# Kernel optimization log

Hardware: AMD Instinct MI355X
Metric: run time of the kernel (lower is better)

## Reference

```python
import jax, jax.numpy as jnp
import numpy as np

B, S, D, H = 2, 2048, 1024, 16
HD = D // H  # head_dim = 64


def setup_inputs() -> dict:
    key = jax.random.key(0)
    ks = jax.random.split(key, 5)
    scale = 1.0 / np.sqrt(D)
    return {
        "x": jax.random.normal(ks[0], (B, S, D), dtype=jnp.float32),
        "attention_mask": jnp.zeros((B, 1, 1, S), dtype=jnp.float32),
        "Wq": jax.random.normal(ks[1], (D, D), dtype=jnp.float32) * scale,
        "Wk": jax.random.normal(ks[2], (D, D), dtype=jnp.float32) * scale,
        "Wv": jax.random.normal(ks[3], (D, D), dtype=jnp.float32) * scale,
        "Wo": jax.random.normal(ks[4], (D, D), dtype=jnp.float32) * scale,
    }


def reference(x, attention_mask, Wq, Wk, Wv, Wo):
    # nn.Linear applies x @ W.T; weights here stored as [out, in]
    q = jnp.einsum("bsd,ed->bse", x, Wq).reshape(B, S, H, HD).transpose(0, 2, 1, 3)
    k = jnp.einsum("bsd,ed->bse", x, Wk).reshape(B, S, H, HD).transpose(0, 2, 1, 3)
    v = jnp.einsum("bsd,ed->bse", x, Wv).reshape(B, S, H, HD).transpose(0, 2, 1, 3)
    scores = jnp.einsum("bhqd,bhkd->bhqk", q, k) / jnp.sqrt(jnp.float32(HD))
    scores = scores + attention_mask  # additive mask, broadcasts [B,1,1,S]
    attn = jax.nn.softmax(scores, axis=-1)  # dropout p=0 (eval) -> identity
    ctx = jnp.einsum("bhqk,bhkd->bhqd", attn, v)
    ctx = ctx.transpose(0, 2, 1, 3).reshape(B, S, D)
    out = jnp.einsum("bsd,ed->bse", ctx, Wo)
    return out
```

## Files before the change

### kernel.cpp

```cpp
#include <hip/hip_runtime.h>
#include <hip/hip_bf16.h>
#include <cstdint>
#include <cstddef>


#define B_  2
#define S_  2048
#define D_  1024
#define H_  16
#define HD_ 64

typedef __bf16 bf16x8 __attribute__((ext_vector_type(8)));
typedef __bf16 bf16x4 __attribute__((ext_vector_type(4)));
typedef float  f32x4  __attribute__((ext_vector_type(4)));

__device__ __forceinline__ void async16(const __bf16* g, const __bf16* l) {
  __builtin_amdgcn_global_load_lds(
      (const __attribute__((address_space(1))) void*)(uintptr_t)g,
      (__attribute__((address_space(3))) void*)(uint32_t)(uintptr_t)l,
      16, 0, 0);
}

__device__ __forceinline__ unsigned cvt_pk_bf16(float lo, float hi) {
  unsigned r;
  asm("v_cvt_pk_bf16_f32 %0, %1, %2" : "=v"(r) : "v"(lo), "v"(hi));
  return r;
}

__global__ __launch_bounds__(256) void cvt_all(const float* __restrict__ x,
    const float* __restrict__ wq, const float* __restrict__ wk,
    const float* __restrict__ wv, const float* __restrict__ wo,
    __bf16* __restrict__ xb, __bf16* __restrict__ wqb, __bf16* __restrict__ wkb,
    __bf16* __restrict__ wvb, __bf16* __restrict__ wob) {
  const int sel = blockIdx.y;
  const float* src; __bf16* dst; int n;
  if      (sel == 0) { src = x;  dst = xb;  n = B_ * S_ * D_; }
  else if (sel == 1) { src = wq; dst = wqb; n = D_ * D_; }
  else if (sel == 2) { src = wk; dst = wkb; n = D_ * D_; }
  else if (sel == 3) { src = wv; dst = wvb; n = D_ * D_; }
  else               { src = wo; dst = wob; n = D_ * D_; }
  for (int i = blockIdx.x * 256 + threadIdx.x; i * 4 < n; i += gridDim.x * 256) {
    const float4 v = *(const float4*)(src + (size_t)i * 4);
    bf16x4 o;
    o[0] = (__bf16)v.x; o[1] = (__bf16)v.y; o[2] = (__bf16)v.z; o[3] = (__bf16)v.w;
    *(bf16x4*)(dst + (size_t)i * 4) = o;
  }
}

template <typename TC>
__device__ __forceinline__ void gemm97_body(const __bf16* __restrict__ A,
                                            const __bf16* __restrict__ Bm,
                                            TC* __restrict__ C,
                                            const int m0, const int n0,
                                            const int N, const int K) {
  __shared__ __align__(16) __bf16 As[128 * 64];
  __shared__ __align__(16) __bf16 Bs[128 * 64];
  const int tid  = threadIdx.x, lane = tid & 63, wave = tid >> 6;
  const int l15  = lane & 15,   quad = lane >> 4;
  const int wr   = wave >> 1,   wc   = wave & 1;
  const int ebase = wave * 2048 + lane * 8;

  f32x4 acc[4][4] = {};
  for (int k0 = 0; k0 < K; k0 += 64) {
#pragma unroll
    for (int i = 0; i < 4; ++i) {
      const int e = ebase + i * 512;
      const int row = e >> 6, col = e & 63;
      async16(A  + (size_t)(m0 + row) * K + k0 + col, As + (wave * 4 + i) * 512);
      async16(Bm + (size_t)(n0 + row) * K + k0 + col, Bs + (wave * 4 + i) * 512);
    }
    __syncthreads();
#pragma unroll
    for (int kk = 0; kk < 2; ++kk) {
      bf16x8 af[4], bfv[4];
#pragma unroll
      for (int rt = 0; rt < 4; ++rt)
        af[rt] = *(const bf16x8*)(As + (wr * 64 + rt * 16 + l15) * 64 + kk * 32 + quad * 8);
#pragma unroll
      for (int ct = 0; ct < 4; ++ct)
        bfv[ct] = *(const bf16x8*)(Bs + (wc * 64 + ct * 16 + l15) * 64 + kk * 32 + quad * 8);
#pragma unroll
      for (int rt = 0; rt < 4; ++rt)
#pragma unroll
        for (int ct = 0; ct < 4; ++ct)
          acc[rt][ct] = __builtin_amdgcn_mfma_f32_16x16x32_bf16(af[rt], bfv[ct], acc[rt][ct], 0, 0, 0);
    }
    __syncthreads();
  }
#pragma unroll
  for (int rt = 0; rt < 4; ++rt)
#pragma unroll
    for (int ct = 0; ct < 4; ++ct)
#pragma unroll
      for (int r = 0; r < 4; ++r) {
        const int row = m0 + wr * 64 + rt * 16 + quad * 4 + r;
        const int col = n0 + wc * 64 + ct * 16 + l15;
        C[(size_t)row * N + col] = (TC)acc[rt][ct][r];
      }
}

__global__ __launch_bounds__(256) void qkv_gemm(const __bf16* __restrict__ xb,
                                                const __bf16* __restrict__ wq,
                                                const __bf16* __restrict__ wk,
                                                const __bf16* __restrict__ wv,
                                                __bf16* __restrict__ qkv) {
  __shared__ __align__(16) __bf16 As[128 * 64];
  __shared__ __align__(16) __bf16 Bs[128 * 64];
  __shared__ __align__(16) __bf16 cs[64 * 136];
  const int sel = blockIdx.x >> 3;
  const __bf16* Bm = (sel == 0) ? wq : (sel == 1) ? wk : wv;
  const int m0 = blockIdx.y * 128, n0 = (blockIdx.x & 7) * 128;
  constexpr int K = D_, N = D_;
  constexpr size_t NTE = (size_t)B_ * S_ * D_;

  const int tid  = threadIdx.x, lane = tid & 63, wave = tid >> 6;
  const int l15  = lane & 15,   quad = lane >> 4;
  const int wr   = wave >> 1,   wc   = wave & 1;
  const int ebase = wave * 2048 + lane * 8;

  f32x4 acc[4][4] = {};
  for (int k0 = 0; k0 < K; k0 += 64) {
#pragma unroll
    for (int i = 0; i < 4; ++i) {
      const int e = ebase + i * 512;
      const int row = e >> 6, col = e & 63;
      async16(xb + (size_t)(m0 + row) * K + k0 + col, As + (wave * 4 + i) * 512);
      async16(Bm + (size_t)(n0 + row) * K + k0 + col, Bs + (wave * 4 + i) * 512);
    }
    __syncthreads();
#pragma unroll
    for (int kk = 0; kk < 2; ++kk) {
      bf16x8 af[4], bfv[4];
#pragma unroll
      for (int rt = 0; rt < 4; ++rt)
        af[rt] = *(const bf16x8*)(As + (wr * 64 + rt * 16 + l15) * 64 + kk * 32 + quad * 8);
#pragma unroll
      for (int ct = 0; ct < 4; ++ct)
        bfv[ct] = *(const bf16x8*)(Bs + (wc * 64 + ct * 16 + l15) * 64 + kk * 32 + quad * 8);
#pragma unroll
      for (int rt = 0; rt < 4; ++rt)
#pragma unroll
        for (int ct = 0; ct < 4; ++ct)
          acc[rt][ct] = __builtin_amdgcn_mfma_f32_16x16x32_bf16(af[rt], bfv[ct], acc[rt][ct], 0, 0, 0);
    }
    __syncthreads();
  }

  const int b  = m0 >> 11;
  const int s0 = m0 & (S_ - 1);
  __bf16* vtb = qkv + 2 * NTE;
#pragma unroll
  for (int pass = 0; pass < 2; ++pass) {
    __syncthreads();
    if (wr == pass) {
#pragma unroll
      for (int rt = 0; rt < 4; ++rt)
#pragma unroll
        for (int ct = 0; ct < 4; ++ct)
#pragma unroll
          for (int r = 0; r < 4; ++r)
            cs[(rt * 16 + quad * 4 + r) * 136 + wc * 64 + ct * 16 + l15] =
                (__bf16)acc[rt][ct][r];
    }
    __syncthreads();
    if (sel < 2) {
      __bf16* C = qkv + (size_t)sel * NTE;
      const int cc = tid & 15, rr = tid >> 4;
#pragma unroll
      for (int p2 = 0; p2 < 4; ++p2) {
        const int row = p2 * 16 + rr;
        const bf16x8 v = *(const bf16x8*)(cs + row * 136 + cc * 8);
        *(bf16x8*)(C + (size_t)(m0 + pass * 64 + row) * N + n0 + cc * 8) = v;
      }
    } else {
      const int e_loc = tid >> 1, sh = (tid & 1) * 32;
      __bf16* dst = vtb + (size_t)(b * 1024 + n0 + e_loc) * S_ + s0 + pass * 64 + sh;
#pragma unroll
      for (int p2 = 0; p2 < 4; ++p2) {
        bf16x8 v;
#pragma unroll
        for (int j = 0; j < 8; ++j)
          v[j] = cs[(sh + p2 * 8 + j) * 136 + e_loc];
        *(bf16x8*)(dst + p2 * 8) = v;
      }
    }
  }
}

__global__ __launch_bounds__(256) void o_gemm(const __bf16* __restrict__ cb,
                                              const __bf16* __restrict__ wo,
                                              float* __restrict__ out) {
  gemm97_body<float>(cb, wo, out, blockIdx.y * 128, blockIdx.x * 128, D_, D_);
}

__global__ __launch_bounds__(512, 4) void attn2(const __bf16* __restrict__ Q,
                                                const __bf16* __restrict__ K,
                                                const __bf16* __restrict__ Vt,
                                                const float* __restrict__ mask,
                                                __bf16* __restrict__ O) {
  constexpr int LKT = 72, LVT = 136;
  __shared__ __align__(16) __bf16 kt[2][128 * LKT];
  __shared__ __align__(16) __bf16 vt[2][64 * LVT];
  __shared__ __align__(16) float  mfull[S_];

  const int tid  = threadIdx.x, lane = tid & 63, wave = tid >> 6;
  const int l15  = lane & 15,   quad = lane >> 4;
  const int b = blockIdx.z, h = blockIdx.y, q0 = blockIdx.x * 128;
  const size_t base   = (size_t)b * S_ * D_ + h * HD_;
  const size_t vtbase = (size_t)(b * H_ + h) * HD_ * S_;
  const int qw = q0 + wave * 16;
  constexpr float LOG2E = 1.44269504088896340736f;
  constexpr float SC    = 0.125f * LOG2E;
  constexpr int  NT     = S_ / 128;

  const int idx0 = tid,        kr0 = idx0 >> 3, kc0 = (idx0 & 7) * 8;
  const int idx1 = 512 + tid,  kr1 = idx1 >> 3, kc1 = (idx1 & 7) * 8;
  const int vr0 = idx0 >> 4, vc0 = (idx0 & 15) * 8;
  const int vr1 = idx1 >> 4, vc1 = (idx1 & 15) * 8;

  bf16x8 qf[2];
#pragma unroll
  for (int kb = 0; kb < 2; ++kb)
    qf[kb] = *(const bf16x8*)(Q + base + (size_t)(qw + l15) * D_ + kb * 32 + quad * 8);

  bf16x8 ones;
#pragma unroll
  for (int j = 0; j < 8; ++j) ones[j] = (__bf16)1.0f;

  float m_run = -1e30f;
  f32x4 oacc[4] = {};
  f32x4 lacc   = {};

  bf16x8 rk0, rk1, rv0, rv1;
  rk0 = *(const bf16x8*)(K + base + (size_t)kr0 * D_ + kc0);
  rk1 = *(const bf16x8*)(K + base + (size_t)kr1 * D_ + kc1);
  rv0 = *(const bf16x8*)(Vt + vtbase + (size_t)vr0 * S_ + vc0);
  rv1 = *(const bf16x8*)(Vt + vtbase + (size_t)vr1 * S_ + vc1);
#pragma unroll
  for (int i = 0; i < S_ / 512; ++i)
    mfull[i * 512 + tid] = mask[(size_t)b * S_ + i * 512 + tid] * LOG2E;
  *(bf16x8*)(&kt[0][kr0 * LKT + kc0]) = rk0;
  *(bf16x8*)(&kt[0][kr1 * LKT + kc1]) = rk1;
  *(bf16x8*)(&vt[0][vr0 * LVT + vc0]) = rv0;
  *(bf16x8*)(&vt[0][vr1 * LVT + vc1]) = rv1;
  __syncthreads();

  for (int t = 0; t < NT; ++t) {
    const int cur = t & 1;
    const int t0  = t * 128;
    const __bf16* ktb = &kt[cur][0];
    const __bf16* vtb = &vt[cur][0];

    if (t + 1 < NT) {
      const int tn = t0 + 128;
      rk0 = *(const bf16x8*)(K + base + (size_t)(tn + kr0) * D_ + kc0);
      rk1 = *(const bf16x8*)(K + base + (size_t)(tn + kr1) * D_ + kc1);
      rv0 = *(const bf16x8*)(Vt + vtbase + (size_t)vr0 * S_ + tn + vc0);
      rv1 = *(const bf16x8*)(Vt + vtbase + (size_t)vr1 * S_ + tn + vc1);
    }

    f32x4 sacc[8] = {};
    __builtin_amdgcn_s_setprio(1);
#pragma unroll
    for (int kti = 0; kti < 8; ++kti) {
      const __bf16* kr = ktb + (kti * 16 + l15) * LKT + quad * 8;
      const bf16x8 a0 = *(const bf16x8*)(kr);
      const bf16x8 a1 = *(const bf16x8*)(kr + 32);
      sacc[kti] = __builtin_amdgcn_mfma_f32_16x16x32_bf16(a0, qf[0], sacc[kti], 0, 0, 0);
      sacc[kti] = __builtin_amdgcn_mfma_f32_16x16x32_bf16(a1, qf[1], sacc[kti], 0, 0, 0);
    }
    __builtin_amdgcn_s_setprio(0);

    f32x4 tm4;
#pragma unroll
    for (int r = 0; r < 4; ++r) tm4[r] = -1e30f;
#pragma unroll
    for (int kti = 0; kti < 8; ++kti) {
      const f32x4 mv = *(const f32x4*)(mfull + t0 + kti * 16 + quad * 4);
#pragma unroll
      for (int r = 0; r < 4; ++r) {
        sacc[kti][r] = sacc[kti][r] * SC + mv[r];
        tm4[r] = fmaxf(tm4[r], sacc[kti][r]);
      }
    }
    float tm = fmaxf(fmaxf(tm4[0], tm4[1]), fmaxf(tm4[2], tm4[3]));
    tm = fmaxf(tm, __shfl_xor(tm, 16));
    tm = fmaxf(tm, __shfl_xor(tm, 32));

    if (!__all(tm <= m_run + 8.f)) {
      const float mnew  = fmaxf(m_run, tm);
      const float alpha = __builtin_amdgcn_exp2f(m_run - mnew);
      m_run = mnew;
#pragma unroll
      for (int r = 0; r < 4; ++r) {
        const float aR = __shfl(alpha, quad * 4 + r);
        lacc[r] *= aR;
#pragma unroll
        for (int nt = 0; nt < 4; ++nt) oacc[nt][r] *= aR;
      }
    }

#pragma unroll
    for (int kb = 0; kb < 4; ++kb) {
      unsigned dd[2][2];
#pragma unroll
      for (int kk = 0; kk < 2; ++kk) {
        const int kti = 2 * kb + kk;
        float p[4];
#pragma unroll
        for (int r = 0; r < 4; ++r)
          p[r] = __builtin_amdgcn_exp2f(sacc[kti][r] - m_run);
        dd[kk][0] = cvt_pk_bf16(p[0], p[1]);
        dd[kk][1] = cvt_pk_bf16(p[2], p[3]);
      }
      unsigned a0 = dd[0][0], b0 = dd[1][0], a1 = dd[0][1], b1 = dd[1][1];
      asm("v_permlane32_swap_b32 %0, %1" : "+v"(a0), "+v"(b0));
      asm("v_permlane16_swap_b32 %0, %1" : "+v"(a0), "+v"(b0));
      asm("v_permlane32_swap_b32 %0, %1" : "+v"(a1), "+v"(b1));
      asm("v_permlane16_swap_b32 %0, %1" : "+v"(a1), "+v"(b1));
      union { unsigned u[4]; bf16x8 v; } pw;
      pw.u[0] = a0; pw.u[1] = a1; pw.u[2] = b0; pw.u[3] = b1;
      const bf16x8 pa = pw.v;
      __builtin_amdgcn_s_setprio(1);
      lacc = __builtin_amdgcn_mfma_f32_16x16x32_bf16(pa, ones, lacc, 0, 0, 0);
#pragma unroll
      for (int nt = 0; nt < 4; ++nt) {
        const bf16x8 vf = *(const bf16x8*)(vtb + (nt * 16 + l15) * LVT + kb * 32 + quad * 8);
        oacc[nt] = __builtin_amdgcn_mfma_f32_16x16x32_bf16(pa, vf, oacc[nt], 0, 0, 0);
      }
      __builtin_amdgcn_s_setprio(0);
    }

    __syncthreads();
    if (t + 1 < NT) {
      const int nxt = cur ^ 1;
      *(bf16x8*)(&kt[nxt][kr0 * LKT + kc0]) = rk0;
      *(bf16x8*)(&kt[nxt][kr1 * LKT + kc1]) = rk1;
      *(bf16x8*)(&vt[nxt][vr0 * LVT + vc0]) = rv0;
      *(bf16x8*)(&vt[nxt][vr1 * LVT + vc1]) = rv1;
    }
    __syncthreads();
  }

#pragma unroll
  for (int r = 0; r < 4; ++r) {
    const float inv = 1.0f / lacc[r];
    const int row = qw + quad * 4 + r;
#pragma unroll
    for (int nt = 0; nt < 4; ++nt)
      O[base + (size_t)row * D_ + nt * 16 + l15] = (__bf16)(oacc[nt][r] * inv);
  }
}

extern "C" void kernel_launch(void* const* d_in, const int* in_sizes, int n_in,
                              void* d_out, int out_size, void* d_ws, size_t ws_size,
                              hipStream_t stream) {
  const float* x    = (const float*)d_in[0];
  const float* mask = (const float*)d_in[1];
  const float* Wq   = (const float*)d_in[2];
  const float* Wk   = (const float*)d_in[3];
  const float* Wv   = (const float*)d_in[4];
  const float* Wo   = (const float*)d_in[5];

  char* ws = (char*)d_ws;
  const size_t MB = 1ull << 20;
  const size_t NT = (size_t)B_ * S_ * D_;
  __bf16* xb  = (__bf16*)(ws);
  __bf16* wqb = (__bf16*)(ws + 8 * MB);
  __bf16* wkb = (__bf16*)(ws + 10 * MB);
  __bf16* wvb = (__bf16*)(ws + 12 * MB);
  __bf16* wob = (__bf16*)(ws + 14 * MB);
  __bf16* qkv = (__bf16*)(ws + 16 * MB);
  __bf16* qb  = qkv;
  __bf16* kb  = qkv + NT;
  __bf16* vtb = qkv + 2 * NT;
  __bf16* cb  = xb;

  cvt_all<<<dim3(1024, 5), 256, 0, stream>>>(x, Wq, Wk, Wv, Wo, xb, wqb, wkb, wvb, wob);
  qkv_gemm<<<dim3(24, 32), 256, 0, stream>>>(xb, wqb, wkb, wvb, qkv);
  attn2<<<dim3(S_ / 128, H_, B_), 512, 0, stream>>>(qb, kb, vtb, mask, cb);
  o_gemm<<<dim3(8, 32), 256, 0, stream>>>(cb, wob, (float*)d_out);
}
```

Measured before the change: 215.0 us.

## Give each attention wave two query tiles and halve o_gemm M tile

The attention kernel now runs 256 threads per block, and each wave handles 32 query rows as two 16-row tiles. Each K and V fragment read from LDS is reused for two sets of MFMAs, and each thread loads four K/V chunks per tile instead of two. This cuts LDS read traffic per unit of work but roughly doubles accumulator registers per wave and reduces the number of waves available to hide latency. Separately, o_gemm switches to 64x128 tiles with twice as many blocks, to fill more compute units for this small GEMM.

```diff
diff --git a/kernel.cpp b/kernel.cpp
--- a/kernel.cpp
+++ b/kernel.cpp
@@ -47,58 +47,6 @@
   }
 }
 
-template <typename TC>
-__device__ __forceinline__ void gemm97_body(const __bf16* __restrict__ A,
-                                            const __bf16* __restrict__ Bm,
-                                            TC* __restrict__ C,
-                                            const int m0, const int n0,
-                                            const int N, const int K) {
-  __shared__ __align__(16) __bf16 As[128 * 64];
-  __shared__ __align__(16) __bf16 Bs[128 * 64];
-  const int tid  = threadIdx.x, lane = tid & 63, wave = tid >> 6;
-  const int l15  = lane & 15,   quad = lane >> 4;
-  const int wr   = wave >> 1,   wc   = wave & 1;
-  const int ebase = wave * 2048 + lane * 8;
-
-  f32x4 acc[4][4] = {};
-  for (int k0 = 0; k0 < K; k0 += 64) {
-#pragma unroll
-    for (int i = 0; i < 4; ++i) {
-      const int e = ebase + i * 512;
-      const int row = e >> 6, col = e & 63;
-      async16(A  + (size_t)(m0 + row) * K + k0 + col, As + (wave * 4 + i) * 512);
-      async16(Bm + (size_t)(n0 + row) * K + k0 + col, Bs + (wave * 4 + i) * 512);
-    }
-    __syncthreads();
-#pragma unroll
-    for (int kk = 0; kk < 2; ++kk) {
-      bf16x8 af[4], bfv[4];
-#pragma unroll
-      for (int rt = 0; rt < 4; ++rt)
-        af[rt] = *(const bf16x8*)(As + (wr * 64 + rt * 16 + l15) * 64 + kk * 32 + quad * 8);
-#pragma unroll
-      for (int ct = 0; ct < 4; ++ct)
-        bfv[ct] = *(const bf16x8*)(Bs + (wc * 64 + ct * 16 + l15) * 64 + kk * 32 + quad * 8);
-#pragma unroll
-      for (int rt = 0; rt < 4; ++rt)
-#pragma unroll
-        for (int ct = 0; ct < 4; ++ct)
-          acc[rt][ct] = __builtin_amdgcn_mfma_f32_16x16x32_bf16(af[rt], bfv[ct], acc[rt][ct], 0, 0, 0);
-    }
-    __syncthreads();
-  }
-#pragma unroll
-  for (int rt = 0; rt < 4; ++rt)
-#pragma unroll
-    for (int ct = 0; ct < 4; ++ct)
-#pragma unroll
-      for (int r = 0; r < 4; ++r) {
-        const int row = m0 + wr * 64 + rt * 16 + quad * 4 + r;
-        const int col = n0 + wc * 64 + ct * 16 + l15;
-        C[(size_t)row * N + col] = (TC)acc[rt][ct][r];
-      }
-}
-
 __global__ __launch_bounds__(256) void qkv_gemm(const __bf16* __restrict__ xb,
                                                 const __bf16* __restrict__ wq,
                                                 const __bf16* __restrict__ wk,
@@ -190,10 +138,59 @@
 __global__ __launch_bounds__(256) void o_gemm(const __bf16* __restrict__ cb,
                                               const __bf16* __restrict__ wo,
                                               float* __restrict__ out) {
-  gemm97_body<float>(cb, wo, out, blockIdx.y * 128, blockIdx.x * 128, D_, D_);
-}
-
-__global__ __launch_bounds__(512, 4) void attn2(const __bf16* __restrict__ Q,
+  __shared__ __align__(16) __bf16 As[64 * 64];
+  __shared__ __align__(16) __bf16 Bs[128 * 64];
+  const int m0 = blockIdx.y * 64, n0 = blockIdx.x * 128;
+  constexpr int K = D_, N = D_;
+  const int tid  = threadIdx.x, lane = tid & 63, wave = tid >> 6;
+  const int l15  = lane & 15,   quad = lane >> 4;
+  const int wr   = wave >> 1,   wc   = wave & 1;
+
+  f32x4 acc[2][4] = {};
+  for (int k0 = 0; k0 < K; k0 += 64) {
+#pragma unroll
+    for (int i = 0; i < 2; ++i) {
+      const int e = i * 2048 + wave * 512 + (lane & 63) * 8;
+      const int row = e >> 6, col = e & 63;
+      async16(cb + (size_t)(m0 + row) * K + k0 + col, As + i * 2048 + wave * 512);
+    }
+#pragma unroll
+    for (int j = 0; j < 4; ++j) {
+      const int e = j * 2048 + wave * 512 + (lane & 63) * 8;
+      const int row = e >> 6, col = e & 63;
+      async16(wo + (size_t)(n0 + row) * K + k0 + col, Bs + j * 2048 + wave * 512);
+    }
+    __syncthreads();
+#pragma unroll
+    for (int kk = 0; kk < 2; ++kk) {
+      bf16x8 af[2], bfv[4];
+#pragma unroll
+      for (int rt = 0; rt < 2; ++rt)
+        af[rt] = *(const bf16x8*)(As + (wr * 32 + rt * 16 + l15) * 64 + kk * 32 + quad * 8);
+#pragma unroll
+      for (int ct = 0; ct < 4; ++ct)
+        bfv[ct] = *(const bf16x8*)(Bs + (wc * 64 + ct * 16 + l15) * 64 + kk * 32 + quad * 8);
+#pragma unroll
+      for (int rt = 0; rt < 2; ++rt)
+#pragma unroll
+        for (int ct = 0; ct < 4; ++ct)
+          acc[rt][ct] = __builtin_amdgcn_mfma_f32_16x16x32_bf16(af[rt], bfv[ct], acc[rt][ct], 0, 0, 0);
+    }
+    __syncthreads();
+  }
+#pragma unroll
+  for (int rt = 0; rt < 2; ++rt)
+#pragma unroll
+    for (int ct = 0; ct < 4; ++ct)
+#pragma unroll
+      for (int r = 0; r < 4; ++r) {
+        const int row = m0 + wr * 32 + rt * 16 + quad * 4 + r;
+        const int col = n0 + wc * 64 + ct * 16 + l15;
+        out[(size_t)row * N + col] = acc[rt][ct][r];
+      }
+}
+
+__global__ __launch_bounds__(256, 2) void attn2(const __bf16* __restrict__ Q,
                                                 const __bf16* __restrict__ K,
                                                 const __bf16* __restrict__ Vt,
                                                 const float* __restrict__ mask,
@@ -208,41 +205,48 @@
   const int b = blockIdx.z, h = blockIdx.y, q0 = blockIdx.x * 128;
   const size_t base   = (size_t)b * S_ * D_ + h * HD_;
   const size_t vtbase = (size_t)(b * H_ + h) * HD_ * S_;
-  const int qw = q0 + wave * 16;
+  const int qw = q0 + wave * 32;
   constexpr float LOG2E = 1.44269504088896340736f;
   constexpr float SC    = 0.125f * LOG2E;
   constexpr int  NT     = S_ / 128;
 
-  const int idx0 = tid,        kr0 = idx0 >> 3, kc0 = (idx0 & 7) * 8;
-  const int idx1 = 512 + tid,  kr1 = idx1 >> 3, kc1 = (idx1 & 7) * 8;
-  const int vr0 = idx0 >> 4, vc0 = (idx0 & 15) * 8;
-  const int vr1 = idx1 >> 4, vc1 = (idx1 & 15) * 8;
-
-  bf16x8 qf[2];
-#pragma unroll
-  for (int kb = 0; kb < 2; ++kb)
-    qf[kb] = *(const bf16x8*)(Q + base + (size_t)(qw + l15) * D_ + kb * 32 + quad * 8);
+  int kr[4], kc[4], vr[4], vc[4];
+#pragma unroll
+  for (int i = 0; i < 4; ++i) {
+    const int idx = i * 256 + tid;
+    kr[i] = idx >> 3;  kc[i] = (idx & 7) * 8;
+    vr[i] = idx >> 4;  vc[i] = (idx & 15) * 8;
+  }
+
+  bf16x8 qf[2][2];
+#pragma unroll
+  for (int t = 0; t < 2; ++t)
+#pragma unroll
+    for (int kb = 0; kb < 2; ++kb)
+      qf[t][kb] = *(const bf16x8*)(Q + base + (size_t)(qw + t * 16 + l15) * D_ + kb * 32 + quad * 8);
 
   bf16x8 ones;
 #pragma unroll
   for (int j = 0; j < 8; ++j) ones[j] = (__bf16)1.0f;
 
-  float m_run = -1e30f;
-  f32x4 oacc[4] = {};
-  f32x4 lacc   = {};
-
-  bf16x8 rk0, rk1, rv0, rv1;
-  rk0 = *(const bf16x8*)(K + base + (size_t)kr0 * D_ + kc0);
-  rk1 = *(const bf16x8*)(K + base + (size_t)kr1 * D_ + kc1);
-  rv0 = *(const bf16x8*)(Vt + vtbase + (size_t)vr0 * S_ + vc0);
-  rv1 = *(const bf16x8*)(Vt + vtbase + (size_t)vr1 * S_ + vc1);
-#pragma unroll
-  for (int i = 0; i < S_ / 512; ++i)
-    mfull[i * 512 + tid] = mask[(size_t)b * S_ + i * 512 + tid] * LOG2E;
-  *(bf16x8*)(&kt[0][kr0 * LKT + kc0]) = rk0;
-  *(bf16x8*)(&kt[0][kr1 * LKT + kc1]) = rk1;
-  *(bf16x8*)(&vt[0][vr0 * LVT + vc0]) = rv0;
-  *(bf16x8*)(&vt[0][vr1 * LVT + vc1]) = rv1;
+  float m_run[2] = {-1e30f, -1e30f};
+  f32x4 oacc[2][4] = {};
+  f32x4 lacc[2]    = {};
+
+  bf16x8 rk[4], rv[4];
+#pragma unroll
+  for (int i = 0; i < 4; ++i) {
+    rk[i] = *(const bf16x8*)(K + base + (size_t)kr[i] * D_ + kc[i]);
+    rv[i] = *(const bf16x8*)(Vt + vtbase + (size_t)vr[i] * S_ + vc[i]);
+  }
+#pragma unroll
+  for (int i = 0; i < S_ / 256; ++i)
+    mfull[i * 256 + tid] = mask[(size_t)b * S_ + i * 256 + tid] * LOG2E;
+#pragma unroll
+  for (int i = 0; i < 4; ++i) {
+    *(bf16x8*)(&kt[0][kr[i] * LKT + kc[i]]) = rk[i];
+    *(bf16x8*)(&vt[0][vr[i] * LVT + vc[i]]) = rv[i];
+  }
   __syncthreads();
 
   for (int t = 0; t < NT; ++t) {
@@ -253,80 +257,98 @@
 
     if (t + 1 < NT) {
       const int tn = t0 + 128;
-      rk0 = *(const bf16x8*)(K + base + (size_t)(tn + kr0) * D_ + kc0);
-      rk1 = *(const bf16x8*)(K + base + (size_t)(tn + kr1) * D_ + kc1);
-      rv0 = *(const bf16x8*)(Vt + vtbase + (size_t)vr0 * S_ + tn + vc0);
-      rv1 = *(const bf16x8*)(Vt + vtbase + (size_t)vr1 * S_ + tn + vc1);
-    }
-
-    f32x4 sacc[8] = {};
+#pragma unroll
+      for (int i = 0; i < 4; ++i) {
+        rk[i] = *(const bf16x8*)(K + base + (size_t)(tn + kr[i]) * D_ + kc[i]);
+        rv[i] = *(const bf16x8*)(Vt + vtbase + (size_t)vr[i] * S_ + tn + vc[i]);
+      }
+    }
+
+    f32x4 sacc[8][2] = {};
     __builtin_amdgcn_s_setprio(1);
 #pragma unroll
     for (int kti = 0; kti < 8; ++kti) {
-      const __bf16* kr = ktb + (kti * 16 + l15) * LKT + quad * 8;
-      const bf16x8 a0 = *(const bf16x8*)(kr);
-      const bf16x8 a1 = *(const bf16x8*)(kr + 32);
-      sacc[kti] = __builtin_amdgcn_mfma_f32_16x16x32_bf16(a0, qf[0], sacc[kti], 0, 0, 0);
-      sacc[kti] = __builtin_amdgcn_mfma_f32_16x16x32_bf16(a1, qf[1], sacc[kti], 0, 0, 0);
+      const __bf16* krp = ktb + (kti * 16 + l15) * LKT + quad * 8;
+      const bf16x8 a0 = *(const bf16x8*)(krp);
+      const bf16x8 a1 = *(const bf16x8*)(krp + 32);
+#pragma unroll
+      for (int tt = 0; tt < 2; ++tt) {
+        sacc[kti][tt] = __builtin_amdgcn_mfma_f32_16x16x32_bf16(a0, qf[tt][0], sacc[kti][tt], 0, 0, 0);
+        sacc[kti][tt] = __builtin_amdgcn_mfma_f32_16x16x32_bf16(a1, qf[tt][1], sacc[kti][tt], 0, 0, 0);
+      }
     }
     __builtin_amdgcn_s_setprio(0);
 
-    f32x4 tm4;
-#pragma unroll
-    for (int r = 0; r < 4; ++r) tm4[r] = -1e30f;
+    f32x4 tm4[2];
+#pragma unroll
+    for (int tt = 0; tt < 2; ++tt)
+#pragma unroll
+      for (int r = 0; r < 4; ++r) tm4[tt][r] = -1e30f;
 #pragma unroll
     for (int kti = 0; kti < 8; ++kti) {
       const f32x4 mv = *(const f32x4*)(mfull + t0 + kti * 16 + quad * 4);
 #pragma unroll
-      for (int r = 0; r < 4; ++r) {
-        sacc[kti][r] = sacc[kti][r] * SC + mv[r];
-        tm4[r] = fmaxf(tm4[r], sacc[kti][r]);
-      }
-    }
-    float tm = fmaxf(fmaxf(tm4[0], tm4[1]), fmaxf(tm4[2], tm4[3]));
-    tm = fmaxf(tm, __shfl_xor(tm, 16));
-    tm = fmaxf(tm, __shfl_xor(tm, 32));
-
-    if (!__all(tm <= m_run + 8.f)) {
-      const float mnew  = fmaxf(m_run, tm);
-      const float alpha = __builtin_amdgcn_exp2f(m_run - mnew);
-      m_run = mnew;
-#pragma unroll
-      for (int r = 0; r < 4; ++r) {
-        const float aR = __shfl(alpha, quad * 4 + r);
-        lacc[r] *= aR;
-#pragma unroll
-        for (int nt = 0; nt < 4; ++nt) oacc[nt][r] *= aR;
+      for (int tt = 0; tt < 2; ++tt)
+#pragma unroll
+        for (int r = 0; r < 4; ++r) {
+          sacc[kti][tt][r] = sacc[kti][tt][r] * SC + mv[r];
+          tm4[tt][r] = fmaxf(tm4[tt][r], sacc[kti][tt][r]);
+        }
+    }
+#pragma unroll
+    for (int tt = 0; tt < 2; ++tt) {
+      float tm = fmaxf(fmaxf(tm4[tt][0], tm4[tt][1]), fmaxf(tm4[tt][2], tm4[tt][3]));
+      tm = fmaxf(tm, __shfl_xor(tm, 16));
+      tm = fmaxf(tm, __shfl_xor(tm, 32));
+      if (!__all(tm <= m_run[tt] + 8.f)) {
+        const float mnew  = fmaxf(m_run[tt], tm);
+        const float alpha = __builtin_amdgcn_exp2f(m_run[tt] - mnew);
+        m_run[tt] = mnew;
+#pragma unroll
+        for (int r = 0; r < 4; ++r) {
+          const float aR = __shfl(alpha, quad * 4 + r);
+          lacc[tt][r] *= aR;
+#pragma unroll
+          for (int nt = 0; nt < 4; ++nt) oacc[tt][nt][r] *= aR;
+        }
       }
     }
 
 #pragma unroll
     for (int kb = 0; kb < 4; ++kb) {
-      unsigned dd[2][2];
-#pragma unroll
-      for (int kk = 0; kk < 2; ++kk) {
-        const int kti = 2 * kb + kk;
-        float p[4];
-#pragma unroll
-        for (int r = 0; r < 4; ++r)
-          p[r] = __builtin_amdgcn_exp2f(sacc[kti][r] - m_run);
-        dd[kk][0] = cvt_pk_bf16(p[0], p[1]);
-        dd[kk][1] = cvt_pk_bf16(p[2], p[3]);
-      }
-      unsigned a0 = dd[0][0], b0 = dd[1][0], a1 = dd[0][1], b1 = dd[1][1];
-      asm("v_permlane32_swap_b32 %0, %1" : "+v"(a0), "+v"(b0));
-      asm("v_permlane16_swap_b32 %0, %1" : "+v"(a0), "+v"(b0));
-      asm("v_permlane32_swap_b32 %0, %1" : "+v"(a1), "+v"(b1));
-      asm("v_permlane16_swap_b32 %0, %1" : "+v"(a1), "+v"(b1));
-      union { unsigned u[4]; bf16x8 v; } pw;
-      pw.u[0] = a0; pw.u[1] = a1; pw.u[2] = b0; pw.u[3] = b1;
-      const bf16x8 pa = pw.v;
+      bf16x8 pa[2];
+#pragma unroll
+      for (int tt = 0; tt < 2; ++tt) {
+        unsigned dd[2][2];
+#pragma unroll
+        for (int kk = 0; kk < 2; ++kk) {
+          const int kti = 2 * kb + kk;
+          float p[4];
+#pragma unroll
+          for (int r = 0; r < 4; ++r)
+            p[r] = __builtin_amdgcn_exp2f(sacc[kti][tt][r] - m_run[tt]);
+          dd[kk][0] = cvt_pk_bf16(p[0], p[1]);
+          dd[kk][1] = cvt_pk_bf16(p[2], p[3]);
+        }
+        unsigned a0 = dd[0][0], b0 = dd[1][0], a1 = dd[0][1], b1 = dd[1][1];
+        asm("v_permlane32_swap_b32 %0, %1" : "+v"(a0), "+v"(b0));
+        asm("v_permlane16_swap_b32 %0, %1" : "+v"(a0), "+v"(b0));
+        asm("v_permlane32_swap_b32 %0, %1" : "+v"(a1), "+v"(b1));
+        asm("v_permlane16_swap_b32 %0, %1" : "+v"(a1), "+v"(b1));
+        union { unsigned u[4]; bf16x8 v; } pw;
+        pw.u[0] = a0; pw.u[1] = a1; pw.u[2] = b0; pw.u[3] = b1;
+        pa[tt] = pw.v;
+      }
       __builtin_amdgcn_s_setprio(1);
-      lacc = __builtin_amdgcn_mfma_f32_16x16x32_bf16(pa, ones, lacc, 0, 0, 0);
+#pragma unroll
+      for (int tt = 0; tt < 2; ++tt)
+        lacc[tt] = __builtin_amdgcn_mfma_f32_16x16x32_bf16(pa[tt], ones, lacc[tt], 0, 0, 0);
 #pragma unroll
       for (int nt = 0; nt < 4; ++nt) {
         const bf16x8 vf = *(const bf16x8*)(vtb + (nt * 16 + l15) * LVT + kb * 32 + quad * 8);
-        oacc[nt] = __builtin_amdgcn_mfma_f32_16x16x32_bf16(pa, vf, oacc[nt], 0, 0, 0);
+#pragma unroll
+        for (int tt = 0; tt < 2; ++tt)
+          oacc[tt][nt] = __builtin_amdgcn_mfma_f32_16x16x32_bf16(pa[tt], vf, oacc[tt][nt], 0, 0, 0);
       }
       __builtin_amdgcn_s_setprio(0);
     }
@@ -334,22 +356,25 @@
     __syncthreads();
     if (t + 1 < NT) {
       const int nxt = cur ^ 1;
-      *(bf16x8*)(&kt[nxt][kr0 * LKT + kc0]) = rk0;
-      *(bf16x8*)(&kt[nxt][kr1 * LKT + kc1]) = rk1;
-      *(bf16x8*)(&vt[nxt][vr0 * LVT + vc0]) = rv0;
-      *(bf16x8*)(&vt[nxt][vr1 * LVT + vc1]) = rv1;
-    }
-    __syncthreads();
-  }
-
-#pragma unroll
-  for (int r = 0; r < 4; ++r) {
-    const float inv = 1.0f / lacc[r];
-    const int row = qw + quad * 4 + r;
-#pragma unroll
-    for (int nt = 0; nt < 4; ++nt)
-      O[base + (size_t)row * D_ + nt * 16 + l15] = (__bf16)(oacc[nt][r] * inv);
-  }
+#pragma unroll
+      for (int i = 0; i < 4; ++i) {
+        *(bf16x8*)(&kt[nxt][kr[i] * LKT + kc[i]]) = rk[i];
+        *(bf16x8*)(&vt[nxt][vr[i] * LVT + vc[i]]) = rv[i];
+      }
+    }
+    __syncthreads();
+  }
+
+#pragma unroll
+  for (int tt = 0; tt < 2; ++tt)
+#pragma unroll
+    for (int r = 0; r < 4; ++r) {
+      const float inv = 1.0f / lacc[tt][r];
+      const int row = qw + tt * 16 + quad * 4 + r;
+#pragma unroll
+      for (int nt = 0; nt < 4; ++nt)
+        O[base + (size_t)row * D_ + nt * 16 + l15] = (__bf16)(oacc[tt][nt][r] * inv);
+    }
 }
 
 extern "C" void kernel_launch(void* const* d_in, const int* in_sizes, int n_in,
@@ -378,6 +403,6 @@
 
   cvt_all<<<dim3(1024, 5), 256, 0, stream>>>(x, Wq, Wk, Wv, Wo, xb, wqb, wkb, wvb, wob);
   qkv_gemm<<<dim3(24, 32), 256, 0, stream>>>(xb, wqb, wkb, wvb, qkv);
-  attn2<<<dim3(S_ / 128, H_, B_), 512, 0, stream>>>(qb, kb, vtb, mask, cb);
-  o_gemm<<<dim3(8, 32), 256, 0, stream>>>(cb, wob, (float*)d_out);
-}
+  attn2<<<dim3(S_ / 128, H_, B_), 256, 0, stream>>>(qb, kb, vtb, mask, cb);
+  o_gemm<<<dim3(8, 64), 256, 0, stream>>>(cb, wob, (float*)d_out);
+}
```

Result: no change. 214.2 us (-0.4%).

## Add XCD-aware block swizzles, shrink o_gemm M-tile, alias LDS in qkv_gemm

Applied to the files above, without the earlier changes.

Remaps block indices in qkv_gemm, o_gemm and attn2 so that blocks landing on the same XCD (round-robin by linear id) share M/N tiles or heads. The aim is better L2 reuse of weights and activations. o_gemm drops to 64-row tiles with twice as many blocks, improving occupancy across the CUs. qkv_gemm now reuses the A/B staging LDS for the epilogue buffer to cut shared memory, and indexes the contiguous wqb/wkb/wvb weights as one fused matrix. That last step relies on the three weight buffers sitting back to back in the workspace (2MB apart).

```diff
diff --git a/kernel.cpp b/kernel.cpp
--- a/kernel.cpp
+++ b/kernel.cpp
@@ -47,14 +47,26 @@
   }
 }
 
-template <typename TC>
-__device__ __forceinline__ void gemm97_body(const __bf16* __restrict__ A,
-                                            const __bf16* __restrict__ Bm,
-                                            TC* __restrict__ C,
-                                            const int m0, const int n0,
-                                            const int N, const int K) {
-  __shared__ __align__(16) __bf16 As[128 * 64];
-  __shared__ __align__(16) __bf16 Bs[128 * 64];
+__global__ __launch_bounds__(256) void qkv_gemm(const __bf16* __restrict__ xb,
+                                                const __bf16* __restrict__ wqkv,
+                                                __bf16* __restrict__ qkv) {
+  __shared__ __align__(16) char smem[32768];
+  __bf16* As = (__bf16*)smem;
+  __bf16* Bs = (__bf16*)(smem + 16384);
+  __bf16* cs = (__bf16*)smem;
+
+  const int lin = blockIdx.y * 24 + blockIdx.x;
+  const int xcd = lin & 7, slot = lin >> 3;
+  const int mi = xcd >> 2, ni = xcd & 3;
+  const int mB = mi * 16 + slot / 6;
+  const int nB = ni * 6  + slot % 6;
+  const int m0  = mB * 128;
+  const int sel = nB >> 3;
+  const int n0s = (nB & 7) * 128;
+  const int n0w = nB * 128;
+  constexpr int K = D_, N = D_;
+  constexpr size_t NTE = (size_t)B_ * S_ * D_;
+
   const int tid  = threadIdx.x, lane = tid & 63, wave = tid >> 6;
   const int l15  = lane & 15,   quad = lane >> 4;
   const int wr   = wave >> 1,   wc   = wave & 1;
@@ -66,8 +78,8 @@
     for (int i = 0; i < 4; ++i) {
       const int e = ebase + i * 512;
       const int row = e >> 6, col = e & 63;
-      async16(A  + (size_t)(m0 + row) * K + k0 + col, As + (wave * 4 + i) * 512);
-      async16(Bm + (size_t)(n0 + row) * K + k0 + col, Bs + (wave * 4 + i) * 512);
+      async16(xb   + (size_t)(m0  + row) * K + k0 + col, As + (wave * 4 + i) * 512);
+      async16(wqkv + (size_t)(n0w + row) * K + k0 + col, Bs + (wave * 4 + i) * 512);
     }
     __syncthreads();
 #pragma unroll
@@ -87,110 +99,106 @@
     }
     __syncthreads();
   }
-#pragma unroll
-  for (int rt = 0; rt < 4; ++rt)
-#pragma unroll
-    for (int ct = 0; ct < 4; ++ct)
-#pragma unroll
-      for (int r = 0; r < 4; ++r) {
-        const int row = m0 + wr * 64 + rt * 16 + quad * 4 + r;
-        const int col = n0 + wc * 64 + ct * 16 + l15;
-        C[(size_t)row * N + col] = (TC)acc[rt][ct][r];
-      }
-}
-
-__global__ __launch_bounds__(256) void qkv_gemm(const __bf16* __restrict__ xb,
-                                                const __bf16* __restrict__ wq,
-                                                const __bf16* __restrict__ wk,
-                                                const __bf16* __restrict__ wv,
-                                                __bf16* __restrict__ qkv) {
-  __shared__ __align__(16) __bf16 As[128 * 64];
+
+  const int b  = m0 >> 11;
+  const int s0 = m0 & (S_ - 1);
+  __bf16* vtb = qkv + 2 * NTE;
+#pragma unroll
+  for (int pass = 0; pass < 2; ++pass) {
+    __syncthreads();
+    if (wr == pass) {
+#pragma unroll
+      for (int rt = 0; rt < 4; ++rt)
+#pragma unroll
+        for (int ct = 0; ct < 4; ++ct)
+#pragma unroll
+          for (int r = 0; r < 4; ++r)
+            cs[(rt * 16 + quad * 4 + r) * 136 + wc * 64 + ct * 16 + l15] =
+                (__bf16)acc[rt][ct][r];
+    }
+    __syncthreads();
+    if (sel < 2) {
+      __bf16* C = qkv + (size_t)sel * NTE;
+      const int cc = tid & 15, rr = tid >> 4;
+#pragma unroll
+      for (int p2 = 0; p2 < 4; ++p2) {
+        const int row = p2 * 16 + rr;
+        const bf16x8 v = *(const bf16x8*)(cs + row * 136 + cc * 8);
+        *(bf16x8*)(C + (size_t)(m0 + pass * 64 + row) * N + n0s + cc * 8) = v;
+      }
+    } else {
+      const int e_loc = tid >> 1, sh = (tid & 1) * 32;
+      __bf16* dst = vtb + (size_t)(b * 1024 + n0s + e_loc) * S_ + s0 + pass * 64 + sh;
+#pragma unroll
+      for (int p2 = 0; p2 < 4; ++p2) {
+        bf16x8 v;
+#pragma unroll
+        for (int j = 0; j < 8; ++j)
+          v[j] = cs[(sh + p2 * 8 + j) * 136 + e_loc];
+        *(bf16x8*)(dst + p2 * 8) = v;
+      }
+    }
+  }
+}
+
+__global__ __launch_bounds__(256) void o_gemm(const __bf16* __restrict__ cb,
+                                              const __bf16* __restrict__ wo,
+                                              float* __restrict__ out) {
+  __shared__ __align__(16) __bf16 As[64 * 64];
   __shared__ __align__(16) __bf16 Bs[128 * 64];
-  __shared__ __align__(16) __bf16 cs[64 * 136];
-  const int sel = blockIdx.x >> 3;
-  const __bf16* Bm = (sel == 0) ? wq : (sel == 1) ? wk : wv;
-  const int m0 = blockIdx.y * 128, n0 = (blockIdx.x & 7) * 128;
+  const int lin = blockIdx.y * 8 + blockIdx.x;
+  const int xcd = lin & 7, slot = lin >> 3;
+  const int mi = xcd >> 1, ni = xcd & 1;
+  const int mB = mi * 16 + (slot >> 2);
+  const int nB = ni * 4  + (slot & 3);
+  const int m0 = mB * 64, n0 = nB * 128;
   constexpr int K = D_, N = D_;
-  constexpr size_t NTE = (size_t)B_ * S_ * D_;
-
   const int tid  = threadIdx.x, lane = tid & 63, wave = tid >> 6;
   const int l15  = lane & 15,   quad = lane >> 4;
   const int wr   = wave >> 1,   wc   = wave & 1;
-  const int ebase = wave * 2048 + lane * 8;
-
-  f32x4 acc[4][4] = {};
+
+  f32x4 acc[2][4] = {};
   for (int k0 = 0; k0 < K; k0 += 64) {
 #pragma unroll
-    for (int i = 0; i < 4; ++i) {
-      const int e = ebase + i * 512;
+    for (int i = 0; i < 2; ++i) {
+      const int e = i * 2048 + wave * 512 + (lane & 63) * 8;
       const int row = e >> 6, col = e & 63;
-      async16(xb + (size_t)(m0 + row) * K + k0 + col, As + (wave * 4 + i) * 512);
-      async16(Bm + (size_t)(n0 + row) * K + k0 + col, Bs + (wave * 4 + i) * 512);
+      async16(cb + (size_t)(m0 + row) * K + k0 + col, As + i * 2048 + wave * 512);
+    }
+#pragma unroll
+    for (int j = 0; j < 4; ++j) {
+      const int e = j * 2048 + wave * 512 + (lane & 63) * 8;
+      const int row = e >> 6, col = e & 63;
+      async16(wo + (size_t)(n0 + row) * K + k0 + col, Bs + j * 2048 + wave * 512);
     }
     __syncthreads();
 #pragma unroll
     for (int kk = 0; kk < 2; ++kk) {
-      bf16x8 af[4], bfv[4];
-#pragma unroll
-      for (int rt = 0; rt < 4; ++rt)
-        af[rt] = *(const bf16x8*)(As + (wr * 64 + rt * 16 + l15) * 64 + kk * 32 + quad * 8);
+      bf16x8 af[2], bfv[4];
+#pragma unroll
+      for (int rt = 0; rt < 2; ++rt)
+        af[rt] = *(const bf16x8*)(As + (wr * 32 + rt * 16 + l15) * 64 + kk * 32 + quad * 8);
 #pragma unroll
       for (int ct = 0; ct < 4; ++ct)
         bfv[ct] = *(const bf16x8*)(Bs + (wc * 64 + ct * 16 + l15) * 64 + kk * 32 + quad * 8);
 #pragma unroll
-      for (int rt = 0; rt < 4; ++rt)
+      for (int rt = 0; rt < 2; ++rt)
 #pragma unroll
         for (int ct = 0; ct < 4; ++ct)
           acc[rt][ct] = __builtin_amdgcn_mfma_f32_16x16x32_bf16(af[rt], bfv[ct], acc[rt][ct], 0, 0, 0);
     }
     __syncthreads();
   }
-
-  const int b  = m0 >> 11;
-  const int s0 = m0 & (S_ - 1);
-  __bf16* vtb = qkv + 2 * NTE;
-#pragma unroll
-  for (int pass = 0; pass < 2; ++pass) {
-    __syncthreads();
-    if (wr == pass) {
-#pragma unroll
-      for (int rt = 0; rt < 4; ++rt)
-#pragma unroll
-        for (int ct = 0; ct < 4; ++ct)
-#pragma unroll
-          for (int r = 0; r < 4; ++r)
-            cs[(rt * 16 + quad * 4 + r) * 136 + wc * 64 + ct * 16 + l15] =
-                (__bf16)acc[rt][ct][r];
-    }
-    __syncthreads();
-    if (sel < 2) {
-      __bf16* C = qkv + (size_t)sel * NTE;
-      const int cc = tid & 15, rr = tid >> 4;
-#pragma unroll
-      for (int p2 = 0; p2 < 4; ++p2) {
-        const int row = p2 * 16 + rr;
-        const bf16x8 v = *(const bf16x8*)(cs + row * 136 + cc * 8);
-        *(bf16x8*)(C + (size_t)(m0 + pass * 64 + row) * N + n0 + cc * 8) = v;
-      }
-    } else {
-      const int e_loc = tid >> 1, sh = (tid & 1) * 32;
-      __bf16* dst = vtb + (size_t)(b * 1024 + n0 + e_loc) * S_ + s0 + pass * 64 + sh;
-#pragma unroll
-      for (int p2 = 0; p2 < 4; ++p2) {
-        bf16x8 v;
-#pragma unroll
-        for (int j = 0; j < 8; ++j)
-          v[j] = cs[(sh + p2 * 8 + j) * 136 + e_loc];
-        *(bf16x8*)(dst + p2 * 8) = v;
-      }
-    }
-  }
-}
-
-__global__ __launch_bounds__(256) void o_gemm(const __bf16* __restrict__ cb,
-                                              const __bf16* __restrict__ wo,
-                                              float* __restrict__ out) {
-  gemm97_body<float>(cb, wo, out, blockIdx.y * 128, blockIdx.x * 128, D_, D_);
+#pragma unroll
+  for (int rt = 0; rt < 2; ++rt)
+#pragma unroll
+    for (int ct = 0; ct < 4; ++ct)
+#pragma unroll
+      for (int r = 0; r < 4; ++r) {
+        const int row = m0 + wr * 32 + rt * 16 + quad * 4 + r;
+        const int col = n0 + wc * 64 + ct * 16 + l15;
+        out[(size_t)row * N + col] = acc[rt][ct][r];
+      }
 }
 
 __global__ __launch_bounds__(512, 4) void attn2(const __bf16* __restrict__ Q,
@@ -205,7 +213,9 @@
 
   const int tid  = threadIdx.x, lane = tid & 63, wave = tid >> 6;
   const int l15  = lane & 15,   quad = lane >> 4;
-  const int b = blockIdx.z, h = blockIdx.y, q0 = blockIdx.x * 128;
+  const int lin = blockIdx.z * 256 + blockIdx.y * 16 + blockIdx.x;
+  const int swz = (lin & 7) * 64 + (lin >> 3);
+  const int b = swz >> 8, h = (swz >> 4) & 15, q0 = (swz & 15) * 128;
   const size_t base   = (size_t)b * S_ * D_ + h * HD_;
   const size_t vtbase = (size_t)(b * H_ + h) * HD_ * S_;
   const int qw = q0 + wave * 16;
@@ -377,7 +387,7 @@
   __bf16* cb  = xb;
 
   cvt_all<<<dim3(1024, 5), 256, 0, stream>>>(x, Wq, Wk, Wv, Wo, xb, wqb, wkb, wvb, wob);
-  qkv_gemm<<<dim3(24, 32), 256, 0, stream>>>(xb, wqb, wkb, wvb, qkv);
+  qkv_gemm<<<dim3(24, 32), 256, 0, stream>>>(xb, wqb, qkv);
   attn2<<<dim3(S_ / 128, H_, B_), 512, 0, stream>>>(qb, kb, vtb, mask, cb);
-  o_gemm<<<dim3(8, 32), 256, 0, stream>>>(cb, wob, (float*)d_out);
-}
+  o_gemm<<<dim3(8, 64), 256, 0, stream>>>(cb, wob, (float*)d_out);
+}
```

New measurement: 210.3 us. -2.2%, faster.
